# Performance work log

Hardware: AMD Instinct MI355X
Metric: run time of the kernel (lower is better)

Reference implementation:

```python
import jax, jax.numpy as jnp
import numpy as np
import math
from jax.ops import segment_sum

TOPK_RATIO = 0.1
CLUSTER_RATIO = 0.25
K_KNN = 10


def setup_inputs() -> dict:
    key = jax.random.key(0)
    ks = jax.random.split(key, 10)
    N, C, H, W = 8, 256, 100, 352
    sc = 0.02
    return {
        "spatial_features_2d": jax.random.normal(ks[0], (N, C, H, W), jnp.float32),
        "dis_priority": jax.random.uniform(ks[1], (N, H, W), dtype=jnp.float32),
        "score_w1": jax.random.normal(ks[2], (256, 256), jnp.float32) * sc,
        "score_b1": jnp.zeros((256,), jnp.float32),
        "score_w2": jax.random.normal(ks[3], (1, 256), jnp.float32) * sc,
        "score_b2": jnp.zeros((1,), jnp.float32),
        "cls_w": jax.random.normal(ks[4], (2, 256), jnp.float32) * sc,
        "cls_b": jnp.zeros((2,), jnp.float32),
        "reg_w": jax.random.normal(ks[5], (14, 256), jnp.float32) * sc,
        "reg_b": jnp.zeros((14,), jnp.float32),
        "record_len": jnp.array([2, 3, 1, 2], jnp.int32),
    }


def _forward(x, dis_priority, score_w1, score_b1, score_w2, score_b2,
             cls_w, cls_b, reg_w, reg_b, record_len):
    N, C, H, W = x.shape
    L = H * W
    xf = x.reshape(N, C, L)  # [N,C,L]

    # --- SortSampler: per-pixel 2-layer fc score net (1x1 convs) ---
    h = jax.nn.relu(jnp.einsum('oc,ncl->nol', score_w1, xf) + score_b1[None, :, None])
    scores = jax.nn.sigmoid(jnp.einsum('oc,ncl->nol', score_w2, h) + score_b2[None, :, None])[:, 0]  # [N,L]
    weight = scores * dis_priority.reshape(N, L)
    K = max(int(math.ceil(L * TOPK_RATIO)), 1)  # static topk token count
    sort_idx = jnp.argsort(-weight, axis=1)[:, :K]              # pos_embed [N,K]
    conf = jnp.take_along_axis(weight, sort_idx, axis=1)        # [N,K]
    feats = jnp.take_along_axis(xf, sort_idx[:, None, :], axis=2)  # [N,C,K]
    src = jnp.transpose(feats, (0, 2, 1)) * conf[:, :, None]    # [N,K,C]

    # --- cluster_dpc_knn ---
    M = max(int(math.ceil(K * CLUSTER_RATIO)), 1)
    sq = jnp.sum(src * src, axis=-1)                             # [N,K]
    dist = sq[:, :, None] + sq[:, None, :] - 2.0 * jnp.einsum('nkc,njc->nkj', src, src)
    dist = jnp.maximum(dist, 0.0)                                # [N,K,K]
    dist_nearest = -jax.lax.top_k(-dist, K_KNN)[0]               # [N,K,k] smallest
    density = jnp.exp(-jnp.mean(dist_nearest, axis=-1))          # [N,K]
    density = density + jnp.arange(K, dtype=density.dtype) * 1e-6  # deterministic tie-break
    higher = density[:, None, :] > density[:, :, None]           # [N,K,K]
    dist_max = jnp.max(dist)
    d_higher = jnp.where(higher, dist, dist_max)
    delta = jnp.min(d_higher, axis=-1)                           # [N,K]
    score = delta * density
    idx_centers = jax.lax.top_k(score, M)[1]                     # [N,M]
    # assign each token to nearest cluster center
    dist_centers = jnp.take_along_axis(dist, idx_centers[:, :, None], axis=1)  # [N,M,K]
    idx_cluster = jnp.argmin(dist_centers, axis=1)               # [N,K]
    idx_cluster = idx_cluster.at[jnp.arange(N)[:, None], idx_centers].set(
        jnp.broadcast_to(jnp.arange(M), (N, M)))

    # --- merge_tokens: weighted average per cluster ---
    flat_seg = (idx_cluster + jnp.arange(N, dtype=idx_cluster.dtype)[:, None] * M).reshape(-1)
    w = conf.reshape(-1)
    all_w = segment_sum(w, flat_seg, num_segments=N * M) + 1e-6          # [N*M]
    merged = segment_sum((src * conf[:, :, None]).reshape(N * K, C), flat_seg,
                         num_segments=N * M) / all_w[:, None]
    merged = merged.reshape(N, M, C)
    # index_points: broadcast merged cluster feature back to each token
    src_tok = jnp.take_along_axis(merged, idx_cluster[:, :, None], axis=1)  # [N,K,C]
    src_ct = jnp.transpose(src_tok, (0, 2, 1))                   # [N,C,K]

    # --- scatter tokens back into BEV grid ---
    def scat(idxs, f):  # idxs [K], f [C,K]
        return jnp.zeros((C, L), f.dtype).at[:, idxs].set(f)
    bev = jax.vmap(scat)(sort_idx, src_ct)                       # [N,C,L]
    # ego CAVs (index 0 within each record) keep the full dense feature
    offsets = jnp.concatenate([jnp.zeros((1,), jnp.int32),
                               jnp.cumsum(record_len)[:-1].astype(jnp.int32)])
    is_ego = jnp.any(jnp.arange(N)[:, None] == offsets[None, :], axis=1)  # [N]
    bev = jnp.where(is_ego[:, None, None], xf, bev).reshape(N, C, H, W)

    # --- ego heads (1x1 convs) ---
    ego = x[offsets]                                              # [B,C,H,W]
    psm_ego = jnp.einsum('oc,bchw->bohw', cls_w, ego) + cls_b[None, :, None, None]
    rm_ego = jnp.einsum('oc,bchw->bohw', reg_w, ego) + reg_b[None, :, None, None]
    return bev, psm_ego, rm_ego


def reference(spatial_features_2d, dis_priority, score_w1, score_b1, score_w2, score_b2,
              cls_w, cls_b, reg_w, reg_b, record_len):
    return _forward(spatial_features_2d, dis_priority, score_w1, score_b1, score_w2,
                    score_b2, cls_w, cls_b, reg_w, reg_b, record_len)
```

## Files before the change

kernel.cpp:

```cpp
#include <hip/hip_runtime.h>
#include <hip/hip_bf16.h>

#define CCH   256
#define LPIX  35200
#define KSEL  3520
#define MCL   880
#define NBINS 16384
#define FMAXV 3.402823466e38f

typedef __bf16 bf16x8 __attribute__((ext_vector_type(8)));
typedef float  f32x4  __attribute__((ext_vector_type(4)));
typedef unsigned short ushort_t;

__device__ __forceinline__ void split3(float v, __bf16* h, __bf16* m, __bf16* l) {
    __bf16 a = (__bf16)v;
    float r = v - (float)a;
    __bf16 b = (__bf16)r;
    float r2 = r - (float)b;
    *h = a; *m = b; *l = (__bf16)r2;
}

__device__ constexpr int SA6[6] = {0, 0, 1, 0, 1, 2};
__device__ constexpr int SB6[6] = {0, 1, 0, 2, 1, 0};

__global__ void split_w1(const float* __restrict__ w1, __bf16* __restrict__ h,
                         __bf16* __restrict__ m, __bf16* __restrict__ l) {
    int i = blockIdx.x * 256 + threadIdx.x;
    split3(w1[i], &h[i], &m[i], &l[i]);
}

__global__ __launch_bounds__(256) void score_mfma(
    const float* __restrict__ x, const float* __restrict__ prio,
    const __bf16* __restrict__ w1h, const __bf16* __restrict__ w1m, const __bf16* __restrict__ w1l,
    const float* __restrict__ b1, const float* __restrict__ w2, const float* __restrict__ b2,
    float* __restrict__ weight, int* __restrict__ hist) {
    int n = blockIdx.y;
    int l0 = blockIdx.x * 64;
    int tid = threadIdx.x, w = tid >> 6, lane = tid & 63;
    int lrow = lane & 15, kg = lane >> 4;
    __shared__ __align__(16) __bf16 Xs[2][3][64][40];
    __shared__ float spart[64][17];
    const float* xb = x + (size_t)n * CCH * LPIX;
    f32x4 acc[4][4];
#pragma unroll
    for (int i = 0; i < 4; i++)
#pragma unroll
        for (int j = 0; j < 4; j++) acc[i][j] = (f32x4){0.f, 0.f, 0.f, 0.f};

    int sl = tid & 63;
    int cg = tid >> 6;

    auto loadx = [&](int k, float* dst) {
        int c0 = k * 32 + cg * 8;
#pragma unroll
        for (int j = 0; j < 8; j++)
            dst[j] = xb[(size_t)(c0 + j) * LPIX + l0 + sl];
    };
    auto loadw = [&](int k, bf16x8* dst) {
#pragma unroll
        for (int fi = 0; fi < 4; fi++) {
            size_t ao = (size_t)(w * 64 + fi * 16 + lrow) * 256 + k * 32 + kg * 8;
            dst[fi * 3 + 0] = *(const bf16x8*)&w1h[ao];
            dst[fi * 3 + 1] = *(const bf16x8*)&w1m[ao];
            dst[fi * 3 + 2] = *(const bf16x8*)&w1l[ao];
        }
    };
    auto stage = [&](int buf, const float* v) {
        bf16x8 vh, vm, vl;
#pragma unroll
        for (int j = 0; j < 8; j++) {
            __bf16 h, m, l;
            split3(v[j], &h, &m, &l);
            vh[j] = h; vm[j] = m; vl[j] = l;
        }
        *(bf16x8*)&Xs[buf][0][sl][cg * 8] = vh;
        *(bf16x8*)&Xs[buf][1][sl][cg * 8] = vm;
        *(bf16x8*)&Xs[buf][2][sl][cg * 8] = vl;
    };

    float pf[2][8];
    bf16x8 wfr[2][12];
    loadx(0, pf[0]);
    loadw(0, wfr[0]);
    stage(0, pf[0]);
    loadx(1, pf[1]);
    __syncthreads();

#pragma unroll
    for (int k = 0; k < 8; k++) {
        const int buf = k & 1;
        bf16x8 bf[3][4];
#pragma unroll
        for (int fj = 0; fj < 4; fj++) {
            bf[0][fj] = *(const bf16x8*)&Xs[buf][0][fj * 16 + lrow][kg * 8];
            bf[1][fj] = *(const bf16x8*)&Xs[buf][1][fj * 16 + lrow][kg * 8];
            bf[2][fj] = *(const bf16x8*)&Xs[buf][2][fj * 16 + lrow][kg * 8];
        }
        if (k < 7) loadw(k + 1, wfr[buf ^ 1]);
        if (k < 6) loadx(k + 2, pf[buf]);
        if (k < 7) stage(buf ^ 1, pf[buf ^ 1]);
#pragma unroll
        for (int t = 0; t < 6; t++) {
#pragma unroll
            for (int fi = 0; fi < 4; fi++) {
#pragma unroll
                for (int fj = 0; fj < 4; fj++) {
                    acc[fi][fj] = __builtin_amdgcn_mfma_f32_16x16x32_bf16(
                        wfr[buf][fi * 3 + SA6[t]], bf[SB6[t]][fj], acc[fi][fj], 0, 0, 0);
                }
            }
        }
        __syncthreads();
    }

    float ps[4] = {0.f, 0.f, 0.f, 0.f};
#pragma unroll
    for (int fi = 0; fi < 4; fi++) {
        int ob = w * 64 + fi * 16 + kg * 4;
        float4 b1v = *(const float4*)&b1[ob];
        float4 w2v = *(const float4*)&w2[ob];
        float b1a[4] = {b1v.x, b1v.y, b1v.z, b1v.w};
        float w2a[4] = {w2v.x, w2v.y, w2v.z, w2v.w};
#pragma unroll
        for (int r = 0; r < 4; r++)
#pragma unroll
            for (int fj = 0; fj < 4; fj++)
                ps[fj] += w2a[r] * fmaxf(acc[fi][fj][r] + b1a[r], 0.f);
    }
#pragma unroll
    for (int fj = 0; fj < 4; fj++) spart[fj * 16 + lrow][w * 4 + kg] = ps[fj];
    __syncthreads();
    if (tid < 64) {
        float s = 0.f;
#pragma unroll
        for (int r = 0; r < 16; r++) s += spart[tid][r];
        s += b2[0];
        float sg = 1.f / (1.f + expf(-s));
        float wv = sg * prio[(size_t)n * LPIX + l0 + tid];
        weight[(size_t)n * LPIX + l0 + tid] = wv;
        int b = (int)(wv * (float)NBINS);
        b = min(max(b, 0), NBINS - 1);
        atomicAdd(&hist[(size_t)n * NBINS + b], 1);
    }
}

__global__ __launch_bounds__(256) void thr_kernel(const int* __restrict__ hist, int* __restrict__ thrbin) {
    int n = blockIdx.x, t = threadIdx.x;
    const int CH = NBINS / 256;
    __shared__ int csum[256];
    __shared__ int bfound;
    int base = NBINS - (t + 1) * CH;
    int s = 0;
    for (int i = 0; i < CH; i++) s += hist[(size_t)n * NBINS + base + i];
    csum[t] = s;
    __syncthreads();
    if (t == 0) {
        int cum = 0, sel = 255;
        for (int u = 0; u < 256; u++) {
            cum += csum[u];
            csum[u] = cum;
            if (cum >= KSEL) { sel = u; break; }
        }
        bfound = sel;
    }
    __syncthreads();
    if (t == 0) {
        int u = bfound;
        int cumBefore = (u == 0) ? 0 : csum[u - 1];
        int base2 = NBINS - (u + 1) * CH;
        int cum = cumBefore, bsel = base2;
        for (int b = base2 + CH - 1; b >= base2; b--) {
            cum += hist[(size_t)n * NBINS + b];
            if (cum >= KSEL) { bsel = b; break; }
        }
        thrbin[n] = bsel;
    }
}

__global__ void cand_kernel(const float* __restrict__ weight, const int* __restrict__ thrbin,
                            float* __restrict__ candw, int* __restrict__ cidx, int* __restrict__ ccnt) {
    int n = blockIdx.y;
    int i = blockIdx.x * 256 + threadIdx.x;
    if (i >= LPIX) return;
    float w = weight[(size_t)n * LPIX + i];
    int b = (int)(w * (float)NBINS);
    b = min(max(b, 0), NBINS - 1);
    if (b >= thrbin[n]) {
        int p = atomicAdd(&ccnt[n], 1);
        candw[(size_t)n * LPIX + p] = w;
        cidx[(size_t)n * LPIX + p] = i;
    }
}

__global__ __launch_bounds__(256) void rank_kernel(const float* __restrict__ candw, const int* __restrict__ cidx,
                                                   const int* __restrict__ ccnt,
                                                   float* __restrict__ conf, int* __restrict__ sidx) {
    int n = blockIdx.y, i = blockIdx.x;
    int cnt = ccnt[n];
    if (i >= cnt) return;
    float wi = candw[(size_t)n * LPIX + i];
    int ii = cidx[(size_t)n * LPIX + i];
    int r = 0;
    for (int j = threadIdx.x; j < cnt; j += 256) {
        float wj = candw[(size_t)n * LPIX + j];
        int ij = cidx[(size_t)n * LPIX + j];
        if (wj > wi || (wj == wi && ij < ii)) r++;
    }
    __shared__ int red[256];
    red[threadIdx.x] = r;
    __syncthreads();
    for (int s = 128; s > 0; s >>= 1) {
        if (threadIdx.x < s) red[threadIdx.x] += red[threadIdx.x + s];
        __syncthreads();
    }
    if (threadIdx.x == 0) {
        int rank = red[0];
        if (rank < KSEL) {
            sidx[(size_t)n * KSEL + rank] = ii;
            conf[(size_t)n * KSEL + rank] = wi;
        }
    }
}

__global__ __launch_bounds__(256) void gather_src(const float* __restrict__ x, const int* __restrict__ sidx,
                                                  const float* __restrict__ conf,
                                                  float* __restrict__ src,
                                                  __bf16* __restrict__ sh, __bf16* __restrict__ sm,
                                                  __bf16* __restrict__ sl,
                                                  float* __restrict__ sq, int* __restrict__ inv) {
    int n = blockIdx.y, k = blockIdx.x, c = threadIdx.x;
    int idx = sidx[(size_t)n * KSEL + k];
    float cf = conf[(size_t)n * KSEL + k];
    float v = x[((size_t)n * CCH + c) * LPIX + idx] * cf;
    size_t o = ((size_t)n * KSEL + k) * CCH + c;
    src[o] = v;
    __bf16 h, m, l;
    split3(v, &h, &m, &l);
    sh[o] = h; sm[o] = m; sl[o] = l;
    __shared__ float red[256];
    red[c] = v * v;
    __syncthreads();
    for (int s = 128; s > 0; s >>= 1) {
        if (c < s) red[c] += red[c + s];
        __syncthreads();
    }
    if (c == 0) {
        sq[(size_t)n * KSEL + k] = red[0];
        inv[(size_t)n * LPIX + idx] = k;
    }
}

__global__ __launch_bounds__(256) void dist_mfma(
    const __bf16* __restrict__ sh, const __bf16* __restrict__ sm, const __bf16* __restrict__ sl,
    const float* __restrict__ sq, float* __restrict__ dist, int n0) {
    int n = n0 + blockIdx.z;
    const size_t nbase = (size_t)n * KSEL * CCH;
    const float* sqn = sq + (size_t)n * KSEL;
    float* D = dist + (size_t)blockIdx.z * KSEL * KSEL;
    int b = blockIdx.x;
    int iT = (int)((sqrtf(8.f * (float)b + 1.f) - 1.f) * 0.5f);
    while ((iT + 1) * (iT + 2) / 2 <= b) iT++;
    while (iT * (iT + 1) / 2 > b) iT--;
    int jT = b - iT * (iT + 1) / 2;
    int bi = iT * 128, bj = jT * 128;
    __shared__ __align__(16) __bf16 As[3][128][40], Bs[3][128][40];
    int tid = threadIdx.x, w = tid >> 6, lane = tid & 63;
    int lrow = lane & 15, kg = lane >> 4;
    int wr = w >> 1, wc = w & 1;
    f32x4 acc[4][4];
#pragma unroll
    for (int i = 0; i < 4; i++)
#pragma unroll
        for (int j = 0; j < 4; j++) acc[i][j] = (f32x4){0.f, 0.f, 0.f, 0.f};

    int sr = tid & 127, g2 = tid >> 7;
    size_t ra = nbase + (size_t)min(bi + sr, KSEL - 1) * CCH;
    size_t rb = nbase + (size_t)min(bj + sr, KSEL - 1) * CCH;

    bf16x8 rA[3][2], rB[3][2];
#pragma unroll
    for (int s2 = 0; s2 < 2; s2++) {
        int cg = s2 * 2 + g2;
        rA[0][s2] = *(const bf16x8*)&sh[ra + cg * 8];
        rA[1][s2] = *(const bf16x8*)&sm[ra + cg * 8];
        rA[2][s2] = *(const bf16x8*)&sl[ra + cg * 8];
        rB[0][s2] = *(const bf16x8*)&sh[rb + cg * 8];
        rB[1][s2] = *(const bf16x8*)&sm[rb + cg * 8];
        rB[2][s2] = *(const bf16x8*)&sl[rb + cg * 8];
    }
    for (int c0 = 0; c0 < 256; c0 += 32) {
        __syncthreads();
#pragma unroll
        for (int s2 = 0; s2 < 2; s2++) {
            int cg = s2 * 2 + g2;
            *(bf16x8*)&As[0][sr][cg * 8] = rA[0][s2];
            *(bf16x8*)&As[1][sr][cg * 8] = rA[1][s2];
            *(bf16x8*)&As[2][sr][cg * 8] = rA[2][s2];
            *(bf16x8*)&Bs[0][sr][cg * 8] = rB[0][s2];
            *(bf16x8*)&Bs[1][sr][cg * 8] = rB[1][s2];
            *(bf16x8*)&Bs[2][sr][cg * 8] = rB[2][s2];
        }
        __syncthreads();
        if (c0 < 224) {
            int c1 = c0 + 32;
#pragma unroll
            for (int s2 = 0; s2 < 2; s2++) {
                int cg = s2 * 2 + g2;
                rA[0][s2] = *(const bf16x8*)&sh[ra + c1 + cg * 8];
                rA[1][s2] = *(const bf16x8*)&sm[ra + c1 + cg * 8];
                rA[2][s2] = *(const bf16x8*)&sl[ra + c1 + cg * 8];
                rB[0][s2] = *(const bf16x8*)&sh[rb + c1 + cg * 8];
                rB[1][s2] = *(const bf16x8*)&sm[rb + c1 + cg * 8];
                rB[2][s2] = *(const bf16x8*)&sl[rb + c1 + cg * 8];
            }
        }
        bf16x8 af[3][4], bf[3][4];
#pragma unroll
        for (int fj = 0; fj < 4; fj++) {
            int brow = wc * 64 + fj * 16 + lrow;
            bf[0][fj] = *(const bf16x8*)&Bs[0][brow][kg * 8];
            bf[1][fj] = *(const bf16x8*)&Bs[1][brow][kg * 8];
            bf[2][fj] = *(const bf16x8*)&Bs[2][brow][kg * 8];
        }
#pragma unroll
        for (int fi = 0; fi < 4; fi++) {
            int arow = wr * 64 + fi * 16 + lrow;
            af[0][fi] = *(const bf16x8*)&As[0][arow][kg * 8];
            af[1][fi] = *(const bf16x8*)&As[1][arow][kg * 8];
            af[2][fi] = *(const bf16x8*)&As[2][arow][kg * 8];
        }
#pragma unroll
        for (int t = 0; t < 6; t++) {
#pragma unroll
            for (int fi = 0; fi < 4; fi++) {
#pragma unroll
                for (int fj = 0; fj < 4; fj++) {
                    acc[fi][fj] = __builtin_amdgcn_mfma_f32_16x16x32_bf16(
                        af[SA6[t]][fi], bf[SB6[t]][fj], acc[fi][fj], 0, 0, 0);
                }
            }
        }
    }
#pragma unroll
    for (int fi = 0; fi < 4; fi++) {
        int gi0 = bi + wr * 64 + fi * 16;
        if (gi0 >= KSEL) continue;
        float4 siv = *(const float4*)&sqn[gi0 + kg * 4];
        float sia[4] = {siv.x, siv.y, siv.z, siv.w};
#pragma unroll
        for (int fj = 0; fj < 4; fj++) {
            int gj0 = bj + wc * 64 + fj * 16;
            if (gj0 >= KSEL) continue;
            int gj = gj0 + lrow;
            float sj = sqn[gj];
            float dv[4];
#pragma unroll
            for (int r = 0; r < 4; r++) {
                int gi = gi0 + kg * 4 + r;
                dv[r] = fmaxf(sia[r] + sj - 2.f * acc[fi][fj][r], 0.f);
                D[(size_t)gi * KSEL + gj] = dv[r];
            }
            if (iT != jT) {
                *(float4*)&D[(size_t)gj * KSEL + gi0 + kg * 4] = *(float4*)dv;
            }
        }
    }
}

__global__ __launch_bounds__(256) void knn_density(const float* __restrict__ dist, float* __restrict__ density, int n0) {
    int n = n0 + blockIdx.y;
    int row = threadIdx.x >> 6;
    int lane = threadIdx.x & 63;
    int i = blockIdx.x * 4 + row;
    const float4* row4 = (const float4*)(dist + (size_t)blockIdx.y * KSEL * KSEL + (size_t)i * KSEL);
    float tt[10];
#pragma unroll
    for (int r = 0; r < 10; r++) tt[r] = FMAXV;
    for (int j4 = lane; j4 < KSEL / 4; j4 += 64) {
        float4 v4 = row4[j4];
        float vv[4] = {v4.x, v4.y, v4.z, v4.w};
#pragma unroll
        for (int q = 0; q < 4; q++) {
            float v = vv[q];
            if (v < tt[9]) {
                tt[9] = v;
#pragma unroll
                for (int r = 9; r > 0; r--) {
                    if (tt[r] < tt[r - 1]) { float tmp = tt[r - 1]; tt[r - 1] = tt[r]; tt[r] = tmp; }
                }
            }
        }
    }
    __shared__ float ls[4][64][10];
#pragma unroll
    for (int r = 0; r < 10; r++) ls[row][lane][r] = tt[r];
    __syncthreads();
    for (int s = 32; s >= 1; s >>= 1) {
        if (lane < s) {
            float out[10];
            int ia = 0, ib = 0;
#pragma unroll
            for (int r = 0; r < 10; r++) {
                float va = ls[row][lane][ia], vb = ls[row][lane + s][ib];
                if (va <= vb) { out[r] = va; ia++; } else { out[r] = vb; ib++; }
            }
#pragma unroll
            for (int r = 0; r < 10; r++) ls[row][lane][r] = out[r];
        }
        __syncthreads();
    }
    if (lane == 0) {
        float sum = 0.f;
#pragma unroll
        for (int r = 0; r < 10; r++) sum += ls[row][0][r];
        density[(size_t)n * KSEL + i] = expf(-sum * 0.1f) + (float)i * 1e-6f;
    }
}

__global__ __launch_bounds__(256) void delta_score(const float* __restrict__ dist, const float* __restrict__ density,
                                                   float* __restrict__ scoreb, int n0) {
    int n = n0 + blockIdx.y;
    int i = blockIdx.x;
    const float4* row = (const float4*)(dist + (size_t)blockIdx.y * KSEL * KSEL + (size_t)i * KSEL);
    const float* dn = density + (size_t)n * KSEL;
    const float4* dn4 = (const float4*)dn;
    float di = dn[i];
    float mn = FMAXV;
    for (int j4 = threadIdx.x; j4 < KSEL / 4; j4 += 256) {
        float4 d = dn4[j4];
        float4 v = row[j4];
        if (d.x > di) mn = fminf(mn, v.x);
        if (d.y > di) mn = fminf(mn, v.y);
        if (d.z > di) mn = fminf(mn, v.z);
        if (d.w > di) mn = fminf(mn, v.w);
    }
    __shared__ float red[256];
    red[threadIdx.x] = mn;
    __syncthreads();
    for (int s = 128; s > 0; s >>= 1) {
        if (threadIdx.x < s) red[threadIdx.x] = fminf(red[threadIdx.x], red[threadIdx.x + s]);
        __syncthreads();
    }
    if (threadIdx.x == 0) {
        float d = red[0];
        scoreb[(size_t)n * KSEL + i] = (d == FMAXV) ? FMAXV : d * di;
    }
}

__global__ __launch_bounds__(256) void center_rank(const float* __restrict__ scoreb, int* __restrict__ centers,
                                                   int* __restrict__ crank, int n0) {
    int n = n0 + blockIdx.y;
    int i = blockIdx.x;
    const float* sc = scoreb + (size_t)n * KSEL;
    float si = sc[i];
    int r = 0;
    for (int j = threadIdx.x; j < KSEL; j += 256) {
        float sj = sc[j];
        if (sj > si || (sj == si && j < i)) r++;
    }
    __shared__ int red[256];
    red[threadIdx.x] = r;
    __syncthreads();
    for (int s = 128; s > 0; s >>= 1) {
        if (threadIdx.x < s) red[threadIdx.x] += red[threadIdx.x + s];
        __syncthreads();
    }
    if (threadIdx.x == 0) {
        int rank = red[0];
        if (rank < MCL) {
            centers[(size_t)n * MCL + rank] = i;
            crank[(size_t)n * KSEL + i] = rank;
        }
    }
}

__global__ __launch_bounds__(256) void assign_kernel(const float* __restrict__ dist, const int* __restrict__ centers,
                                                     const int* __restrict__ crank, const float* __restrict__ conf,
                                                     int* __restrict__ clus, float* __restrict__ allw, int n0) {
    int n = n0 + blockIdx.y;
    const float* D = dist + (size_t)blockIdx.y * KSEL * KSEL;
    int kl = threadIdx.x & 63, mc = threadIdx.x >> 6;
    int k = blockIdx.x * 64 + kl;
    const int* ctr = centers + (size_t)n * MCL;
    float mn = FMAXV;
    int am = MCL;
    for (int m = mc * 220; m < (mc + 1) * 220; m++) {
        float v = D[(size_t)ctr[m] * KSEL + k];
        if (v < mn) { mn = v; am = m; }
    }
    __shared__ float mv[4][64];
    __shared__ int mi[4][64];
    mv[mc][kl] = mn;
    mi[mc][kl] = am;
    __syncthreads();
    if (mc == 0) {
        float best = mv[0][kl];
        int bm = mi[0][kl];
#pragma unroll
        for (int c = 1; c < 4; c++) {
            float v = mv[c][kl];
            int im = mi[c][kl];
            if (v < best || (v == best && im < bm)) { best = v; bm = im; }
        }
        int cr = crank[(size_t)n * KSEL + k];
        int cl = (cr >= 0) ? cr : bm;
        clus[(size_t)n * KSEL + k] = cl;
        atomicAdd(&allw[(size_t)n * MCL + cl], conf[(size_t)n * KSEL + k]);
    }
}

__global__ void merge_feat(const float* __restrict__ src, const float* __restrict__ conf,
                           const int* __restrict__ clus, float* __restrict__ merged, int n0) {
    int n = n0 + blockIdx.y;
    int k = blockIdx.x, c = threadIdx.x;
    float v = src[((size_t)n * KSEL + k) * CCH + c] * conf[(size_t)n * KSEL + k];
    atomicAdd(&merged[((size_t)n * MCL + clus[(size_t)n * KSEL + k]) * CCH + c], v);
}

__global__ void merged_div(float* __restrict__ merged, const float* __restrict__ allw) {
    int nm = blockIdx.x, c = threadIdx.x;
    merged[(size_t)nm * CCH + c] /= (allw[nm] + 1e-6f);
}

__global__ __launch_bounds__(256) void bev_kernel(const float* __restrict__ x, const int* __restrict__ inv,
                                                  const int* __restrict__ clus, const float* __restrict__ merged,
                                                  const int* __restrict__ reclen, int B,
                                                  const float* __restrict__ clsw, const float* __restrict__ clsb,
                                                  const float* __restrict__ regw, const float* __restrict__ regb,
                                                  float* __restrict__ out, float* __restrict__ psm,
                                                  float* __restrict__ rm) {
    int n = blockIdx.y;
    int l0 = (blockIdx.x * 256 + threadIdx.x) * 4;
    bool ego = false;
    int bego = 0;
    {
        int off = 0;
        for (int b = 0; b < B; b++) {
            if (n == off) { ego = true; bego = b; break; }
            off += reclen[b];
        }
    }
    __shared__ float ws[16][256];
    __shared__ float bs[16];
    if (ego) {
        for (int i = threadIdx.x; i < 16 * 256; i += 256) {
            int o = i >> 8, c = i & 255;
            ws[o][c] = (o < 2) ? clsw[o * 256 + c] : regw[(o - 2) * 256 + c];
        }
        if (threadIdx.x < 16) bs[threadIdx.x] = (threadIdx.x < 2) ? clsb[threadIdx.x] : regb[threadIdx.x - 2];
        __syncthreads();
    }
    if (l0 >= LPIX) return;
    size_t base = (size_t)n * CCH * LPIX + l0;
    if (ego) {
        float acc[16][4] = {};
        for (int c = 0; c < CCH; c++) {
            float4 v = *(const float4*)&x[base + (size_t)c * LPIX];
            *(float4*)&out[base + (size_t)c * LPIX] = v;
#pragma unroll
            for (int o = 0; o < 16; o++) {
                float wv = ws[o][c];
                acc[o][0] += wv * v.x; acc[o][1] += wv * v.y; acc[o][2] += wv * v.z; acc[o][3] += wv * v.w;
            }
        }
#pragma unroll
        for (int o = 0; o < 2; o++) {
            float4 r;
            r.x = acc[o][0] + bs[o]; r.y = acc[o][1] + bs[o]; r.z = acc[o][2] + bs[o]; r.w = acc[o][3] + bs[o];
            *(float4*)&psm[((size_t)bego * 2 + o) * LPIX + l0] = r;
        }
#pragma unroll
        for (int o = 0; o < 14; o++) {
            float4 r;
            float bb = bs[o + 2];
            r.x = acc[o + 2][0] + bb; r.y = acc[o + 2][1] + bb; r.z = acc[o + 2][2] + bb; r.w = acc[o + 2][3] + bb;
            *(float4*)&rm[((size_t)bego * 14 + o) * LPIX + l0] = r;
        }
    } else {
        const float* mr0; const float* mr1; const float* mr2; const float* mr3;
        {
            int t0 = inv[(size_t)n * LPIX + l0 + 0];
            int t1 = inv[(size_t)n * LPIX + l0 + 1];
            int t2 = inv[(size_t)n * LPIX + l0 + 2];
            int t3 = inv[(size_t)n * LPIX + l0 + 3];
            mr0 = (t0 >= 0) ? merged + ((size_t)n * MCL + clus[(size_t)n * KSEL + t0]) * CCH : nullptr;
            mr1 = (t1 >= 0) ? merged + ((size_t)n * MCL + clus[(size_t)n * KSEL + t1]) * CCH : nullptr;
            mr2 = (t2 >= 0) ? merged + ((size_t)n * MCL + clus[(size_t)n * KSEL + t2]) * CCH : nullptr;
            mr3 = (t3 >= 0) ? merged + ((size_t)n * MCL + clus[(size_t)n * KSEL + t3]) * CCH : nullptr;
        }
        for (int c = 0; c < CCH; c++) {
            float4 v;
            v.x = mr0 ? mr0[c] : 0.f;
            v.y = mr1 ? mr1[c] : 0.f;
            v.z = mr2 ? mr2[c] : 0.f;
            v.w = mr3 ? mr3[c] : 0.f;
            *(float4*)&out[base + (size_t)c * LPIX] = v;
        }
    }
}

extern "C" void kernel_launch(void* const* d_in, const int* in_sizes, int n_in,
                              void* d_out, int out_size, void* d_ws, size_t ws_size,
                              hipStream_t stream) {
    const float* x    = (const float*)d_in[0];
    const float* prio = (const float*)d_in[1];
    const float* w1   = (const float*)d_in[2];
    const float* b1   = (const float*)d_in[3];
    const float* w2   = (const float*)d_in[4];
    const float* b2   = (const float*)d_in[5];
    const float* clsw = (const float*)d_in[6];
    const float* clsb = (const float*)d_in[7];
    const float* regw = (const float*)d_in[8];
    const float* regb = (const float*)d_in[9];
    const int* reclen = (const int*)d_in[10];
    int N = in_sizes[0] / (CCH * LPIX);
    int B = in_sizes[10];
    float* out = (float*)d_out;

    char* p = (char*)d_ws;
    size_t off = 0;
    auto alloc = [&](size_t bytes) -> void* {
        void* r = p + off;
        off += (bytes + 255) & ~(size_t)255;
        return r;
    };
    __bf16* w1h    = (__bf16*)alloc(256 * 256 * 2);
    __bf16* w1m    = (__bf16*)alloc(256 * 256 * 2);
    __bf16* w1l    = (__bf16*)alloc(256 * 256 * 2);
    float* weight  = (float*)alloc((size_t)N * LPIX * 4);
    int*   hist    = (int*)alloc((size_t)N * NBINS * 4);
    int*   thrbin  = (int*)alloc((size_t)N * 4);
    int*   ccnt    = (int*)alloc((size_t)N * 4);
    float* candw   = (float*)alloc((size_t)N * LPIX * 4);
    int*   cidx    = (int*)alloc((size_t)N * LPIX * 4);
    int*   sidx    = (int*)alloc((size_t)N * KSEL * 4);
    float* conf    = (float*)alloc((size_t)N * KSEL * 4);
    float* src     = (float*)alloc((size_t)N * KSEL * CCH * 4);
    __bf16* srch   = (__bf16*)alloc((size_t)N * KSEL * CCH * 2);
    __bf16* srcm   = (__bf16*)alloc((size_t)N * KSEL * CCH * 2);
    __bf16* srcl   = (__bf16*)alloc((size_t)N * KSEL * CCH * 2);
    float* sq      = (float*)alloc((size_t)N * KSEL * 4);
    int*   inv     = (int*)alloc((size_t)N * LPIX * 4);
    float* density = (float*)alloc((size_t)N * KSEL * 4);
    float* scoreb  = (float*)alloc((size_t)N * KSEL * 4);
    int*   centers = (int*)alloc((size_t)N * MCL * 4);
    int*   crank   = (int*)alloc((size_t)N * KSEL * 4);
    int*   clus    = (int*)alloc((size_t)N * KSEL * 4);
    float* allw    = (float*)alloc((size_t)N * MCL * 4);
    float* merged  = (float*)alloc((size_t)N * MCL * CCH * 4);
    const size_t distB = (size_t)KSEL * KSEL * 4;
    size_t rem = (ws_size > off) ? (ws_size - off) : 0;
    int nd = (int)(rem / distB);
    if (nd < 1) nd = 1;
    if (nd > N) nd = N;
    float* dist = (float*)alloc(distB * nd);

    hipMemsetAsync(hist, 0, (size_t)N * NBINS * 4, stream);
    hipMemsetAsync(ccnt, 0, (size_t)N * 4, stream);
    hipMemsetAsync(inv, 0xFF, (size_t)N * LPIX * 4, stream);
    hipMemsetAsync(crank, 0xFF, (size_t)N * KSEL * 4, stream);
    hipMemsetAsync(allw, 0, (size_t)N * MCL * 4, stream);
    hipMemsetAsync(merged, 0, (size_t)N * MCL * CCH * 4, stream);

    split_w1<<<256, 256, 0, stream>>>(w1, w1h, w1m, w1l);
    score_mfma<<<dim3(LPIX / 64, N), 256, 0, stream>>>(x, prio, w1h, w1m, w1l, b1, w2, b2, weight, hist);
    thr_kernel<<<N, 256, 0, stream>>>(hist, thrbin);
    cand_kernel<<<dim3((LPIX + 255) / 256, N), 256, 0, stream>>>(weight, thrbin, candw, cidx, ccnt);
    rank_kernel<<<dim3(8192, N), 256, 0, stream>>>(candw, cidx, ccnt, conf, sidx);
    gather_src<<<dim3(KSEL, N), 256, 0, stream>>>(x, sidx, conf, src, srch, srcm, srcl, sq, inv);

    const int TI = (KSEL + 127) / 128;
    const int NT = TI * (TI + 1) / 2;
    for (int g = 0; g < N; g += nd) {
        int nb = (N - g < nd) ? (N - g) : nd;
        dist_mfma<<<dim3(NT, 1, nb), 256, 0, stream>>>(srch, srcm, srcl, sq, dist, g);
        knn_density<<<dim3(KSEL / 4, nb), 256, 0, stream>>>(dist, density, g);
        delta_score<<<dim3(KSEL, nb), 256, 0, stream>>>(dist, density, scoreb, g);
        center_rank<<<dim3(KSEL, nb), 256, 0, stream>>>(scoreb, centers, crank, g);
        assign_kernel<<<dim3(KSEL / 64, nb), 256, 0, stream>>>(dist, centers, crank, conf, clus, allw, g);
        merge_feat<<<dim3(KSEL, nb), 256, 0, stream>>>(src, conf, clus, merged, g);
    }
    merged_div<<<N * MCL, 256, 0, stream>>>(merged, allw);

    float* psm = out + (size_t)N * CCH * LPIX;
    float* rm  = psm + (size_t)B * 2 * LPIX;
    bev_kernel<<<dim3((LPIX / 4 + 255) / 256, N), 256, 0, stream>>>(
        x, inv, clus, merged, reclen, B, clsw, clsb, regw, regb, out, psm, rm);
}
```

Before: 1.297 ms.

## Widen score GEMM K-stage to 64 channels and remap dist blocks by XCD

The score kernel now stages 64 channels per iteration instead of 32, halving the number of barrier-separated stages. W1 fragments are loaded per 32-channel sub-step directly before use rather than double-buffered in registers, which lowers register pressure. The LDS tile grows accordingly. Separately, the dist kernel remaps the triangular block index so that consecutive tiles land on the same XCD, aiming for better L2 locality of the shared rows. The trade-offs are more LDS per block and W1 load latency that is no longer prefetched.

```diff
diff --git a/kernel.cpp b/kernel.cpp
--- a/kernel.cpp
+++ b/kernel.cpp
@@ -38,7 +38,7 @@
     int l0 = blockIdx.x * 64;
     int tid = threadIdx.x, w = tid >> 6, lane = tid & 63;
     int lrow = lane & 15, kg = lane >> 4;
-    __shared__ __align__(16) __bf16 Xs[2][3][64][40];
+    __shared__ __align__(16) __bf16 Xs[2][3][64][72];
     __shared__ float spart[64][17];
     const float* xb = x + (size_t)n * CCH * LPIX;
     f32x4 acc[4][4];
@@ -51,62 +51,66 @@
     int cg = tid >> 6;
 
     auto loadx = [&](int k, float* dst) {
-        int c0 = k * 32 + cg * 8;
-#pragma unroll
-        for (int j = 0; j < 8; j++)
-            dst[j] = xb[(size_t)(c0 + j) * LPIX + l0 + sl];
-    };
-    auto loadw = [&](int k, bf16x8* dst) {
-#pragma unroll
-        for (int fi = 0; fi < 4; fi++) {
-            size_t ao = (size_t)(w * 64 + fi * 16 + lrow) * 256 + k * 32 + kg * 8;
-            dst[fi * 3 + 0] = *(const bf16x8*)&w1h[ao];
-            dst[fi * 3 + 1] = *(const bf16x8*)&w1m[ao];
-            dst[fi * 3 + 2] = *(const bf16x8*)&w1l[ao];
-        }
+        int c0 = k * 64;
+#pragma unroll
+        for (int h = 0; h < 2; h++)
+#pragma unroll
+            for (int j = 0; j < 8; j++)
+                dst[h * 8 + j] = xb[(size_t)(c0 + (cg + 4 * h) * 8 + j) * LPIX + l0 + sl];
     };
     auto stage = [&](int buf, const float* v) {
-        bf16x8 vh, vm, vl;
-#pragma unroll
-        for (int j = 0; j < 8; j++) {
-            __bf16 h, m, l;
-            split3(v[j], &h, &m, &l);
-            vh[j] = h; vm[j] = m; vl[j] = l;
-        }
-        *(bf16x8*)&Xs[buf][0][sl][cg * 8] = vh;
-        *(bf16x8*)&Xs[buf][1][sl][cg * 8] = vm;
-        *(bf16x8*)&Xs[buf][2][sl][cg * 8] = vl;
+#pragma unroll
+        for (int h = 0; h < 2; h++) {
+            bf16x8 vh, vm, vl;
+#pragma unroll
+            for (int j = 0; j < 8; j++) {
+                __bf16 hh, mm, ll;
+                split3(v[h * 8 + j], &hh, &mm, &ll);
+                vh[j] = hh; vm[j] = mm; vl[j] = ll;
+            }
+            *(bf16x8*)&Xs[buf][0][sl][(cg + 4 * h) * 8] = vh;
+            *(bf16x8*)&Xs[buf][1][sl][(cg + 4 * h) * 8] = vm;
+            *(bf16x8*)&Xs[buf][2][sl][(cg + 4 * h) * 8] = vl;
+        }
     };
 
-    float pf[2][8];
-    bf16x8 wfr[2][12];
+    float pf[2][16];
     loadx(0, pf[0]);
-    loadw(0, wfr[0]);
     stage(0, pf[0]);
     loadx(1, pf[1]);
     __syncthreads();
 
 #pragma unroll
-    for (int k = 0; k < 8; k++) {
+    for (int k = 0; k < 4; k++) {
         const int buf = k & 1;
-        bf16x8 bf[3][4];
-#pragma unroll
-        for (int fj = 0; fj < 4; fj++) {
-            bf[0][fj] = *(const bf16x8*)&Xs[buf][0][fj * 16 + lrow][kg * 8];
-            bf[1][fj] = *(const bf16x8*)&Xs[buf][1][fj * 16 + lrow][kg * 8];
-            bf[2][fj] = *(const bf16x8*)&Xs[buf][2][fj * 16 + lrow][kg * 8];
-        }
-        if (k < 7) loadw(k + 1, wfr[buf ^ 1]);
-        if (k < 6) loadx(k + 2, pf[buf]);
-        if (k < 7) stage(buf ^ 1, pf[buf ^ 1]);
-#pragma unroll
-        for (int t = 0; t < 6; t++) {
+        if (k < 3) stage(buf ^ 1, pf[buf ^ 1]);
+        if (k < 2) loadx(k + 2, pf[buf]);
+#pragma unroll
+        for (int kk = 0; kk < 2; kk++) {
+            const int cbase = k * 64 + kk * 32;
+            bf16x8 bf[3][4], af[3][4];
+#pragma unroll
+            for (int fj = 0; fj < 4; fj++) {
+                bf[0][fj] = *(const bf16x8*)&Xs[buf][0][fj * 16 + lrow][kk * 32 + kg * 8];
+                bf[1][fj] = *(const bf16x8*)&Xs[buf][1][fj * 16 + lrow][kk * 32 + kg * 8];
+                bf[2][fj] = *(const bf16x8*)&Xs[buf][2][fj * 16 + lrow][kk * 32 + kg * 8];
+            }
 #pragma unroll
             for (int fi = 0; fi < 4; fi++) {
-#pragma unroll
-                for (int fj = 0; fj < 4; fj++) {
-                    acc[fi][fj] = __builtin_amdgcn_mfma_f32_16x16x32_bf16(
-                        wfr[buf][fi * 3 + SA6[t]], bf[SB6[t]][fj], acc[fi][fj], 0, 0, 0);
+                size_t ao = (size_t)(w * 64 + fi * 16 + lrow) * 256 + cbase + kg * 8;
+                af[0][fi] = *(const bf16x8*)&w1h[ao];
+                af[1][fi] = *(const bf16x8*)&w1m[ao];
+                af[2][fi] = *(const bf16x8*)&w1l[ao];
+            }
+#pragma unroll
+            for (int t = 0; t < 6; t++) {
+#pragma unroll
+                for (int fi = 0; fi < 4; fi++) {
+#pragma unroll
+                    for (int fj = 0; fj < 4; fj++) {
+                        acc[fi][fj] = __builtin_amdgcn_mfma_f32_16x16x32_bf16(
+                            af[SA6[t]][fi], bf[SB6[t]][fj], acc[fi][fj], 0, 0, 0);
+                    }
                 }
             }
         }
@@ -257,7 +261,9 @@
     const size_t nbase = (size_t)n * KSEL * CCH;
     const float* sqn = sq + (size_t)n * KSEL;
     float* D = dist + (size_t)blockIdx.z * KSEL * KSEL;
-    int b = blockIdx.x;
+    int orig = blockIdx.x;
+    int xcd = orig & 7, loc = orig >> 3;
+    int b = (xcd < 6 ? xcd * 51 : 306 + (xcd - 6) * 50) + loc;
     int iT = (int)((sqrtf(8.f * (float)b + 1.f) - 1.f) * 0.5f);
     while ((iT + 1) * (iT + 2) / 2 <= b) iT++;
     while (iT * (iT + 1) / 2 > b) iT--;
```

Result: no change. 1.293 ms (-0.3%).
